# Kernel tuning notes

Measured on AMD Instinct MI355X. Metric: run time of the kernel, lower is better.

## Reference

```python
import jax, jax.numpy as jnp
import numpy as np

N, E, F_IN, F_OUT = 16384, 4096, 128, 128
EPS = 1e-6


def setup_inputs() -> dict:
    key = jax.random.key(0)
    k1, k2, k3 = jax.random.split(key, 3)
    H = (jax.random.uniform(k1, (N, E)) < 0.05).astype(jnp.float32)
    x = jax.random.normal(k2, (N, F_IN), dtype=jnp.float32)
    W = jax.random.normal(k3, (F_IN, F_OUT), dtype=jnp.float32) * 0.05
    return {"x": x, "H": H, "W": W}


def reference(x, H, W):
    # D_v^{-1} H D_e^{-1} H^T x W, computed without materializing the NxN
    # adjacency: diagonal matmuls become row/col broadcast scaling, and the
    # GEMM chain is reordered right-to-left (same math, associativity).
    d_e_inv = 1.0 / (H.sum(axis=0) + EPS)   # [E]
    d_v_inv = 1.0 / (H.sum(axis=1) + EPS)   # [N]
    xw = x @ W                               # [N, F_out]
    edge_msg = H.T @ xw                      # [E, F_out] gather onto edges
    edge_msg = d_e_inv[:, None] * edge_msg   # D_e^{-1}
    node_msg = H @ edge_msg                  # [N, F_out] scatter back to nodes
    return d_v_inv[:, None] * node_msg       # D_v^{-1}
```

## Files before the change

### kernel.cpp

```cpp
#include <hip/hip_runtime.h>
#include <stdint.h>

#define N_NODES 16384
#define N_EDGES 4096
#define FDIM    128
#define EPSF    1e-6f
#define NPAIRS  64

typedef __attribute__((ext_vector_type(8))) short short8;
typedef __attribute__((ext_vector_type(4))) float f32x4;
typedef unsigned long long ull;

__device__ __forceinline__ unsigned short f2bf(float f) {
    uint32_t u = __float_as_uint(f);
    return (unsigned short)((u + 0x7FFFu + ((u >> 16) & 1u)) >> 16);
}
__device__ __forceinline__ short8 as_s8(uint4 v) {
    union { uint4 a; short8 b; } u; u.a = v; return u.b;
}

__device__ __forceinline__ short8 expand8(uint32_t half, int bitoff) {
    uint32_t b8 = (half >> bitoff) & 0xFFu;
    uint32_t lo = ((b8 & 0xFu) * 0x00204081u) & 0x01010101u;
    uint32_t hi = ((b8 >> 4) * 0x00204081u) & 0x01010101u;
    union { short8 v; uint32_t u[4]; } a;
#if __has_builtin(__builtin_amdgcn_perm)
    a.u[0] = __builtin_amdgcn_perm(0u, lo, 0x04010400u) * 0x3F80u;
    a.u[1] = __builtin_amdgcn_perm(0u, lo, 0x04030402u) * 0x3F80u;
    a.u[2] = __builtin_amdgcn_perm(0u, hi, 0x04010400u) * 0x3F80u;
    a.u[3] = __builtin_amdgcn_perm(0u, hi, 0x04030402u) * 0x3F80u;
#else
    a.u[0] = ((lo & 1u)         | ((lo >> 8) & 1u) << 16) * 0x3F80u;
    a.u[1] = (((lo >> 16) & 1u) | ((lo >> 24) & 1u) << 16) * 0x3F80u;
    a.u[2] = ((hi & 1u)         | ((hi >> 8) & 1u) << 16) * 0x3F80u;
    a.u[3] = (((hi >> 16) & 1u) | ((hi >> 24) & 1u) << 16) * 0x3F80u;
#endif
    return a.v;
}

__device__ __forceinline__ ull bit_transpose64(ull q, int lane) {
    const ull M32 = 0xFFFFFFFF00000000ull, M16 = 0xFFFF0000FFFF0000ull,
              M8 = 0xFF00FF00FF00FF00ull, M4 = 0xF0F0F0F0F0F0F0F0ull,
              M2 = 0xCCCCCCCCCCCCCCCCull, M1 = 0xAAAAAAAAAAAAAAAAull;
#define TSTEP(d, Md) { ull tv = __shfl_xor(q, d, 64); \
    q = ((lane & d) == 0) ? ((q & ~Md) | ((tv << d) & Md)) \
                          : ((q & Md) | ((tv >> d) & ~Md)); }
    TSTEP(32, M32) TSTEP(16, M16) TSTEP(8, M8) TSTEP(4, M4) TSTEP(2, M2) TSTEP(1, M1)
#undef TSTEP
    return q;
}

__global__ __launch_bounds__(256) void k_bitpack(const float* __restrict__ H,
        ull* __restrict__ bitsNE, float* __restrict__ dvinv) {
    int w = threadIdx.x >> 6, lane = threadIdx.x & 63;
    int n = blockIdx.x * 4 + w;
    const float4* hr = (const float4*)(H + (size_t)n * N_EDGES);
    ull* out = bitsNE + (size_t)n * (N_EDGES / 64);
    int cnt = 0;
    for (int c4 = 0; c4 < N_EDGES / 256; ++c4) {
        float4 v = hr[c4 * 64 + lane];
        ull b0 = __ballot(v.x > 0.5f);
        ull b1 = __ballot(v.y > 0.5f);
        ull b2 = __ballot(v.z > 0.5f);
        ull b3 = __ballot(v.w > 0.5f);
        cnt += __popcll(b0) + __popcll(b1) + __popcll(b2) + __popcll(b3);
        if (lane == 0) {
            #pragma unroll
            for (int q = 0; q < 4; ++q) {
                ull wq = ((b0 >> (16 * q)) & 0xFFFFull)
                       | (((b1 >> (16 * q)) & 0xFFFFull) << 16)
                       | (((b2 >> (16 * q)) & 0xFFFFull) << 32)
                       | (((b3 >> (16 * q)) & 0xFFFFull) << 48);
                out[c4 * 4 + q] = wq;
            }
        }
    }
    if (lane == 0) dvinv[n] = 1.0f / ((float)cnt + EPSF);
}

__global__ __launch_bounds__(256) void k_transpose_bf(const ull* __restrict__ bitsNE,
        ull* __restrict__ bitsEN) {
    int w = threadIdx.x >> 6, lane = threadIdx.x & 63;
    int wid = blockIdx.x * 4 + w;
    int nt = wid >> 3, etg = wid & 7;
    int pl = 4 * (lane & 15) + (lane >> 4);
    const ull* src = bitsNE + (size_t)(nt * 64 + pl) * (N_EDGES / 64);
    #pragma unroll
    for (int i = 0; i < 8; ++i) {
        int et = etg * 8 + i;
        ull q = src[et];
        q = bit_transpose64(q, lane);
        bitsEN[(size_t)(et * 64 + pl) * (N_NODES / 64) + nt] = q;
    }
}

__global__ __launch_bounds__(256) void k_edeg(const ull* __restrict__ bitsEN,
        float* __restrict__ deinv) {
    int w = threadIdx.x >> 6, lane = threadIdx.x & 63;
    int e = blockIdx.x * 4 + w;
    const ull* r = bitsEN + (size_t)e * (N_NODES / 64);
    int s = __popcll(r[lane]) + __popcll(r[lane + 64]) + __popcll(r[lane + 128]) + __popcll(r[lane + 192]);
    for (int o = 32; o; o >>= 1) s += __shfl_xor(s, o);
    if (lane == 0) deinv[e] = 1.0f / ((float)s + EPSF);
}

__global__ __launch_bounds__(256) void k_xw(const float* __restrict__ x, const float* __restrict__ W,
        unsigned short* __restrict__ xwTp) {
    __shared__ __attribute__((aligned(16))) unsigned short ldsWT[128 * 136];
    __shared__ __attribute__((aligned(16))) unsigned short ldsT[128 * 72];
    int t = threadIdx.x, lane = t & 63, w = t >> 6;
    int r16 = lane & 15, klane = lane >> 4;
    for (int i = 0; i < 64; ++i) {
        int idx = i * 256 + t;
        int k = idx >> 7, f = idx & 127;
        ldsWT[f * 136 + k] = f2bf(W[idx]);
    }
    __syncthreads();
    int nbase = blockIdx.x * 64;
    int row = nbase + w * 16 + r16;
    const float4* xr4 = (const float4*)(x + (size_t)row * FDIM);
    f32x4 acc[8] = {};
    for (int kb = 0; kb < 128; kb += 32) {
        float4 u0 = xr4[(kb >> 2) + klane * 2];
        float4 u1 = xr4[(kb >> 2) + klane * 2 + 1];
        union { short8 v; unsigned short u[8]; } a;
        a.u[0] = f2bf(u0.x); a.u[1] = f2bf(u0.y); a.u[2] = f2bf(u0.z); a.u[3] = f2bf(u0.w);
        a.u[4] = f2bf(u1.x); a.u[5] = f2bf(u1.y); a.u[6] = f2bf(u1.z); a.u[7] = f2bf(u1.w);
        #pragma unroll
        for (int fb = 0; fb < 8; ++fb) {
            short8 b = *(const short8*)&ldsWT[(fb * 16 + r16) * 136 + kb + klane * 8];
            acc[fb] = __builtin_amdgcn_mfma_f32_16x16x32_bf16(a.v, b, acc[fb], 0, 0, 0);
        }
    }
    #pragma unroll
    for (int fb = 0; fb < 8; ++fb)
        #pragma unroll
        for (int r = 0; r < 4; ++r)
            ldsT[(fb * 16 + r16) * 72 + 16 * r + w * 4 + klane] = f2bf(acc[fb][r]);
    __syncthreads();
    int f = t >> 1, part = t & 1;
    #pragma unroll
    for (int j = 0; j < 4; ++j)
        *(uint4*)&xwTp[(size_t)f * N_NODES + nbase + part * 32 + j * 8] =
            *(const uint4*)&ldsT[f * 72 + part * 32 + j * 8];
}

#define LOADP(Q0, Q1, BUF, p) do { \
    Q0 = brow0[(p)]; Q1 = brow1[(p)]; \
    const unsigned short* _src = bcol + (size_t)(p) * 64; \
    _Pragma("unroll") \
    for (int _fb = 0; _fb < 4; ++_fb) { \
        BUF[_fb * 2]     = *(const uint4*)(_src + _fb * fbstride); \
        BUF[_fb * 2 + 1] = *(const uint4*)(_src + _fb * fbstride + 32); \
    } } while (0)

#define COMPUTEP(Q0, Q1, BUF) do { \
    _Pragma("unroll") \
    for (int _s2 = 0; _s2 < 2; ++_s2) { \
        uint32_t _h0 = (uint32_t)(_s2 == 0 ? (Q0) : ((Q0) >> 32)); \
        uint32_t _h1 = (uint32_t)(_s2 == 0 ? (Q1) : ((Q1) >> 32)); \
        short8 _a0 = expand8(_h0, bitoff); \
        short8 _a1 = expand8(_h1, bitoff); \
        _Pragma("unroll") \
        for (int _f = 0; _f < 4; ++_f) { \
            short8 _b = as_s8(BUF[_f * 2 + _s2]); \
            acc[0][_f] = __builtin_amdgcn_mfma_f32_16x16x32_bf16(_a0, _b, acc[0][_f], 0, 0, 0); \
            acc[1][_f] = __builtin_amdgcn_mfma_f32_16x16x32_bf16(_a1, _b, acc[1][_f], 0, 0, 0); \
        } } } while (0)

template<bool FINAL>
__global__ __launch_bounds__(256) void k_gemm_gen(
        const ull* __restrict__ bits, int krows,
        const unsigned short* __restrict__ BT, int K,
        float* __restrict__ Cout, const float* __restrict__ rowScale, int M) {
    int t = threadIdx.x, lane = t & 63, w = t >> 6;
    int r16 = lane & 15, klane = lane >> 4;
    int bitoff = klane * 8;
    int wm = w >> 1, wf = w & 1;
    int mbase = blockIdx.x * 64 + wm * 32;
    int kq0 = blockIdx.z * NPAIRS;
    const ull* brow0 = bits + (size_t)(mbase + r16) * krows + kq0;
    const ull* brow1 = brow0 + (size_t)16 * krows;
    const unsigned short* bcol = BT + (size_t)(wf * 64 + r16) * K + (size_t)kq0 * 64 + klane * 8;
    const size_t fbstride = (size_t)16 * K;
    f32x4 acc[2][4] = {};
    ull qA0, qA1, qB0, qB1, qC0, qC1;
    uint4 bufA[8], bufB[8], bufC[8];
    LOADP(qA0, qA1, bufA, 0);
    LOADP(qB0, qB1, bufB, 1);
    LOADP(qC0, qC1, bufC, 2);
    for (int p = 0; p <= NPAIRS - 7; p += 3) {
        COMPUTEP(qA0, qA1, bufA); LOADP(qA0, qA1, bufA, p + 3);
        COMPUTEP(qB0, qB1, bufB); LOADP(qB0, qB1, bufB, p + 4);
        COMPUTEP(qC0, qC1, bufC); LOADP(qC0, qC1, bufC, p + 5);
    }
    COMPUTEP(qA0, qA1, bufA); LOADP(qA0, qA1, bufA, NPAIRS - 1);
    COMPUTEP(qB0, qB1, bufB);
    COMPUTEP(qC0, qC1, bufC);
    COMPUTEP(qA0, qA1, bufA);
    #pragma unroll
    for (int fr = 0; fr < 2; ++fr)
        #pragma unroll
        for (int fb = 0; fb < 4; ++fb)
            #pragma unroll
            for (int r = 0; r < 4; ++r) {
                int row = mbase + fr * 16 + klane * 4 + r;
                int col = wf * 64 + fb * 16 + r16;
                float v = acc[fr][fb][r];
                if (FINAL)
                    Cout[(size_t)row * FDIM + col] = rowScale[row] * v;
                else
                    Cout[(size_t)blockIdx.z * M * FDIM + (size_t)row * FDIM + col] = v;
            }
}

__global__ __launch_bounds__(256) void k_reduce_scale_T(const float* __restrict__ partials,
        const float* __restrict__ deinv, unsigned short* __restrict__ emTp, int S) {
    __shared__ float lds[64 * 129];
    int t = threadIdx.x;
    int e0 = blockIdx.x * 64;
    for (int i = 0; i < 32; ++i) {
        int idx = i * 256 + t;
        int e_l = idx >> 7, f = idx & 127;
        float s = 0.f;
        for (int z = 0; z < S; ++z)
            s += partials[(size_t)z * N_EDGES * FDIM + (size_t)(e0 + e_l) * FDIM + f];
        lds[e_l * 129 + f] = s * deinv[e0 + e_l];
    }
    __syncthreads();
    for (int i = 0; i < 32; ++i) {
        int idx = i * 256 + t;
        int f = idx >> 6, j = idx & 63;
        int pj = 4 * (j & 15) + (j >> 4);
        emTp[(size_t)f * N_EDGES + e0 + j] = f2bf(lds[pj * 129 + f]);
    }
}

extern "C" void kernel_launch(void* const* d_in, const int* in_sizes, int n_in,
                              void* d_out, int out_size, void* d_ws, size_t ws_size,
                              hipStream_t stream) {
    const float* x = (const float*)d_in[0];
    const float* H = (const float*)d_in[1];
    const float* W = (const float*)d_in[2];
    float* out = (float*)d_out;
    char* ws = (char*)d_ws;

    ull* bitsNE = (ull*)(ws);
    ull* bitsEN = (ull*)(ws + (8u << 20));
    unsigned short* xwTp = (unsigned short*)(ws + (16u << 20));
    unsigned short* emTp = (unsigned short*)(ws + (20u << 20));
    float* dvinv = (float*)(ws + (21u << 20));
    float* deinv = (float*)(ws + (21u << 20) + 65536);
    float* partE = (float*)(ws + (22u << 20));

    hipLaunchKernelGGL(k_bitpack, dim3(4096), dim3(256), 0, stream, H, bitsNE, dvinv);
    hipLaunchKernelGGL(k_transpose_bf, dim3(512), dim3(256), 0, stream, bitsNE, bitsEN);
    hipLaunchKernelGGL(k_edeg, dim3(1024), dim3(256), 0, stream, bitsEN, deinv);
    hipLaunchKernelGGL(k_xw, dim3(256), dim3(256), 0, stream, x, W, xwTp);
    hipLaunchKernelGGL((k_gemm_gen<false>), dim3(64, 1, 4), dim3(256), 0, stream,
                       bitsEN, N_NODES / 64, xwTp, N_NODES, partE, (const float*)nullptr,
                       N_EDGES);
    hipLaunchKernelGGL(k_reduce_scale_T, dim3(64), dim3(256), 0, stream, partE, deinv, emTp, 4);
    hipLaunchKernelGGL((k_gemm_gen<true>), dim3(256, 1, 1), dim3(256), 0, stream,
                       bitsNE, N_EDGES / 64, emTp, N_EDGES, out, dvinv,
                       N_NODES);
}
```

Measured before the change: 250.3 us.

## Increase split-K factor for both bit-packed GEMMs and add partial-sum reduction

Makes the K-chunk length a template parameter. The edge GEMM is split 8 ways instead of 4, and the node GEMM is now split 2 ways, writing partials that a new elementwise kernel sums and scales by the inverse vertex degree. This raises grid size so more CUs are busy, since 64 and 256 blocks underfill the GPU. In exchange it adds extra partial-buffer traffic and one more kernel launch. The new path runs only when the workspace is large enough.

```diff
diff --git a/kernel.cpp b/kernel.cpp
--- a/kernel.cpp
+++ b/kernel.cpp
@@ -5,7 +5,6 @@
 #define N_EDGES 4096
 #define FDIM    128
 #define EPSF    1e-6f
-#define NPAIRS  64
 
 typedef __attribute__((ext_vector_type(8))) short short8;
 typedef __attribute__((ext_vector_type(4))) float f32x4;
@@ -168,17 +167,18 @@
             acc[1][_f] = __builtin_amdgcn_mfma_f32_16x16x32_bf16(_a1, _b, acc[1][_f], 0, 0, 0); \
         } } } while (0)
 
-template<bool FINAL>
+template<bool FINAL, int NP>
 __global__ __launch_bounds__(256) void k_gemm_gen(
         const ull* __restrict__ bits, int krows,
         const unsigned short* __restrict__ BT, int K,
         float* __restrict__ Cout, const float* __restrict__ rowScale, int M) {
+    static_assert(NP % 3 == 1 || NP % 3 == 2, "tail requires NP%3 in {1,2}");
     int t = threadIdx.x, lane = t & 63, w = t >> 6;
     int r16 = lane & 15, klane = lane >> 4;
     int bitoff = klane * 8;
     int wm = w >> 1, wf = w & 1;
     int mbase = blockIdx.x * 64 + wm * 32;
-    int kq0 = blockIdx.z * NPAIRS;
+    int kq0 = blockIdx.z * NP;
     const ull* brow0 = bits + (size_t)(mbase + r16) * krows + kq0;
     const ull* brow1 = brow0 + (size_t)16 * krows;
     const unsigned short* bcol = BT + (size_t)(wf * 64 + r16) * K + (size_t)kq0 * 64 + klane * 8;
@@ -189,15 +189,23 @@
     LOADP(qA0, qA1, bufA, 0);
     LOADP(qB0, qB1, bufB, 1);
     LOADP(qC0, qC1, bufC, 2);
-    for (int p = 0; p <= NPAIRS - 7; p += 3) {
+    for (int p = 0; p <= NP - 7; p += 3) {
         COMPUTEP(qA0, qA1, bufA); LOADP(qA0, qA1, bufA, p + 3);
         COMPUTEP(qB0, qB1, bufB); LOADP(qB0, qB1, bufB, p + 4);
         COMPUTEP(qC0, qC1, bufC); LOADP(qC0, qC1, bufC, p + 5);
     }
-    COMPUTEP(qA0, qA1, bufA); LOADP(qA0, qA1, bufA, NPAIRS - 1);
-    COMPUTEP(qB0, qB1, bufB);
-    COMPUTEP(qC0, qC1, bufC);
-    COMPUTEP(qA0, qA1, bufA);
+    if constexpr (NP % 3 == 1) {
+        COMPUTEP(qA0, qA1, bufA); LOADP(qA0, qA1, bufA, NP - 1);
+        COMPUTEP(qB0, qB1, bufB);
+        COMPUTEP(qC0, qC1, bufC);
+        COMPUTEP(qA0, qA1, bufA);
+    } else {
+        COMPUTEP(qA0, qA1, bufA); LOADP(qA0, qA1, bufA, NP - 2);
+        COMPUTEP(qB0, qB1, bufB); LOADP(qB0, qB1, bufB, NP - 1);
+        COMPUTEP(qC0, qC1, bufC);
+        COMPUTEP(qA0, qA1, bufA);
+        COMPUTEP(qB0, qB1, bufB);
+    }
     #pragma unroll
     for (int fr = 0; fr < 2; ++fr)
         #pragma unroll
@@ -236,6 +244,22 @@
     }
 }
 
+__global__ __launch_bounds__(256) void k_finalN(const float* __restrict__ partN,
+        const float* __restrict__ dvinv, float* __restrict__ out) {
+    const float4* pa = (const float4*)partN;
+    const float4* pb = (const float4*)(partN + (size_t)N_NODES * FDIM);
+    float4* o4 = (float4*)out;
+    int t = threadIdx.x;
+    #pragma unroll
+    for (int i = 0; i < 4; ++i) {
+        int idx = blockIdx.x * 1024 + i * 256 + t;
+        float4 a = pa[idx], b = pb[idx];
+        float s = dvinv[idx >> 5];
+        o4[idx] = make_float4((a.x + b.x) * s, (a.y + b.y) * s,
+                              (a.z + b.z) * s, (a.w + b.w) * s);
+    }
+}
+
 extern "C" void kernel_launch(void* const* d_in, const int* in_sizes, int n_in,
                               void* d_out, int out_size, void* d_ws, size_t ws_size,
                               hipStream_t stream) {
@@ -252,16 +276,30 @@
     float* dvinv = (float*)(ws + (21u << 20));
     float* deinv = (float*)(ws + (21u << 20) + 65536);
     float* partE = (float*)(ws + (22u << 20));
+    float* partN = (float*)(ws + (38u << 20));
+
+    bool big = ws_size >= ((38u << 20) + (size_t)2 * N_NODES * FDIM * 4);
 
     hipLaunchKernelGGL(k_bitpack, dim3(4096), dim3(256), 0, stream, H, bitsNE, dvinv);
     hipLaunchKernelGGL(k_transpose_bf, dim3(512), dim3(256), 0, stream, bitsNE, bitsEN);
     hipLaunchKernelGGL(k_edeg, dim3(1024), dim3(256), 0, stream, bitsEN, deinv);
     hipLaunchKernelGGL(k_xw, dim3(256), dim3(256), 0, stream, x, W, xwTp);
-    hipLaunchKernelGGL((k_gemm_gen<false>), dim3(64, 1, 4), dim3(256), 0, stream,
-                       bitsEN, N_NODES / 64, xwTp, N_NODES, partE, (const float*)nullptr,
-                       N_EDGES);
-    hipLaunchKernelGGL(k_reduce_scale_T, dim3(64), dim3(256), 0, stream, partE, deinv, emTp, 4);
-    hipLaunchKernelGGL((k_gemm_gen<true>), dim3(256, 1, 1), dim3(256), 0, stream,
-                       bitsNE, N_EDGES / 64, emTp, N_EDGES, out, dvinv,
-                       N_NODES);
-}
+    if (big) {
+        hipLaunchKernelGGL((k_gemm_gen<false, 32>), dim3(64, 1, 8), dim3(256), 0, stream,
+                           bitsEN, N_NODES / 64, xwTp, N_NODES, partE, (const float*)nullptr,
+                           N_EDGES);
+        hipLaunchKernelGGL(k_reduce_scale_T, dim3(64), dim3(256), 0, stream, partE, deinv, emTp, 8);
+        hipLaunchKernelGGL((k_gemm_gen<false, 32>), dim3(256, 1, 2), dim3(256), 0, stream,
+                           bitsNE, N_EDGES / 64, emTp, N_EDGES, partN, (const float*)nullptr,
+                           N_NODES);
+        hipLaunchKernelGGL(k_finalN, dim3(512), dim3(256), 0, stream, partN, dvinv, out);
+    } else {
+        hipLaunchKernelGGL((k_gemm_gen<false, 64>), dim3(64, 1, 4), dim3(256), 0, stream,
+                           bitsEN, N_NODES / 64, xwTp, N_NODES, partE, (const float*)nullptr,
+                           N_EDGES);
+        hipLaunchKernelGGL(k_reduce_scale_T, dim3(64), dim3(256), 0, stream, partE, deinv, emTp, 4);
+        hipLaunchKernelGGL((k_gemm_gen<true, 64>), dim3(256, 1, 1), dim3(256), 0, stream,
+                           bitsNE, N_EDGES / 64, emTp, N_EDGES, out, dvinv,
+                           N_NODES);
+    }
+}
```

After: 293.3 us. 1.17x slower.
